# Performance work log

Hardware: AMD Instinct MI355X
Metric: run time of the kernel (lower is better)

The kernel has to match this reference:

```python
import jax, jax.numpy as jnp
import numpy as np

N, E = 20000, 320000
NODE_DIM, EDGE_DIM, EMB, HEADS, HIDDEN, OUT = 128, 16, 128, 4, 512, 64
NEG_SLOPE = 0.2


def _gatv2(x, src0, dst0, ea, Wl, bl, Wr, br, We, att, bias):
    """PyG GATv2Conv (concat=True, add_self_loops=True, fill_value='mean')."""
    n = x.shape[0]
    e = src0.shape[0]
    H, C = att.shape
    # self loops; self-loop edge_attr = mean of incoming edge_attr per node (0 if none)
    cnt = jax.ops.segment_sum(jnp.ones((e,), x.dtype), dst0, num_segments=n)
    loop_attr = jax.ops.segment_sum(ea, dst0, num_segments=n) / jnp.maximum(cnt, 1.0)[:, None]
    loops = jnp.arange(n, dtype=src0.dtype)
    src = jnp.concatenate([src0, loops])
    dst = jnp.concatenate([dst0, loops])
    ea_full = jnp.concatenate([ea, loop_attr], axis=0)
    xl = (x @ Wl + bl).reshape(n, H, C)   # source transform
    xr = (x @ Wr + br).reshape(n, H, C)   # target transform
    ef = (ea_full @ We).reshape(-1, H, C)  # edge transform (no bias in PyG)
    s = jax.nn.leaky_relu(xl[src] + xr[dst] + ef, NEG_SLOPE)  # [E', H, C]
    logits = jnp.einsum('ehc,hc->eh', s, att)
    # scatter-softmax over incoming edges of each dst node (stable)
    mx = jax.ops.segment_max(logits, dst, num_segments=n)
    num = jnp.exp(logits - mx[dst])
    den = jax.ops.segment_sum(num, dst, num_segments=n)
    alpha = num / (den[dst] + 1e-16)
    out = jax.ops.segment_sum(alpha[:, :, None] * xl[src], dst, num_segments=n)
    return out.reshape(n, H * C) + bias


def _lin(key, fan_in, fan_out, dt=jnp.float32):
    return jax.random.normal(key, (fan_in, fan_out), dt) * (1.0 / np.sqrt(fan_in))


def setup_inputs() -> dict:
    key = jax.random.key(0)
    ks = jax.random.split(key, 24)
    HC = HEADS * EMB
    inp = {
        'x': jax.random.normal(ks[0], (N, NODE_DIM), jnp.float32),
        'edge_index': jax.random.randint(ks[1], (2, E), 0, N, jnp.int64),
        'edge_attr': jax.random.normal(ks[2], (E, EDGE_DIM), jnp.float32),
        # GATv2 layer 1
        'Wl1': _lin(ks[3], NODE_DIM, HC), 'bl1': jnp.zeros((HC,), jnp.float32),
        'Wr1': _lin(ks[4], NODE_DIM, HC), 'br1': jnp.zeros((HC,), jnp.float32),
        'We1': _lin(ks[5], EDGE_DIM, HC),
        'att1': jax.random.normal(ks[6], (HEADS, EMB), jnp.float32) * (1.0 / np.sqrt(EMB)),
        'bias1': jnp.zeros((HC,), jnp.float32),
        # GATv2 layer 2
        'Wl2': _lin(ks[7], HC, HC), 'bl2': jnp.zeros((HC,), jnp.float32),
        'Wr2': _lin(ks[8], HC, HC), 'br2': jnp.zeros((HC,), jnp.float32),
        'We2': _lin(ks[9], EDGE_DIM, HC),
        'att2': jax.random.normal(ks[10], (HEADS, EMB), jnp.float32) * (1.0 / np.sqrt(EMB)),
        'bias2': jnp.zeros((HC,), jnp.float32),
        # decoder MLP
        'Wd1': _lin(ks[11], HC, HIDDEN), 'bd1': jnp.zeros((HIDDEN,), jnp.float32),
        'Wd2': _lin(ks[12], HIDDEN, OUT), 'bd2': jnp.zeros((OUT,), jnp.float32),
    }
    return inp


def reference(x, edge_index, edge_attr,
              Wl1, bl1, Wr1, br1, We1, att1, bias1,
              Wl2, bl2, Wr2, br2, We2, att2, bias2,
              Wd1, bd1, Wd2, bd2):
    src, dst = edge_index[0], edge_index[1]
    h = _gatv2(x, src, dst, edge_attr, Wl1, bl1, Wr1, br1, We1, att1, bias1)
    h = _gatv2(h, src, dst, edge_attr, Wl2, bl2, Wr2, br2, We2, att2, bias2)
    q = jax.nn.relu(h @ Wd1 + bd1) @ Wd2 + bd2
    return q
```

## Files before the change

### kernel.cpp

```cpp
#include <hip/hip_runtime.h>
#include <hip/hip_fp16.h>

typedef _Float16 half8 __attribute__((ext_vector_type(8)));
typedef _Float16 half2v __attribute__((ext_vector_type(2)));
typedef float f32x4 __attribute__((ext_vector_type(4)));

#if __has_builtin(__builtin_amdgcn_fdot2)
#define FDOT2(a, b, c) __builtin_amdgcn_fdot2((a), (b), (c), false)
#else
static __device__ __forceinline__ float FDOT2(half2v a, half2v b, float c) {
  return (float)a[0] * (float)b[0] + (float)a[1] * (float)b[1] + c;
}
#endif
#define H2(v8, p) ((half2v){(v8)[2 * (p)], (v8)[2 * (p) + 1]})

#define GLOAD_LDS16(gp, lp)                                                        \
  __builtin_amdgcn_global_load_lds(                                                \
      (const __attribute__((address_space(1))) void*)(gp),                         \
      (__attribute__((address_space(3))) void*)(lp), 16, 0, 0)

template <int CTRL>
__device__ __forceinline__ float dpp_add16(float x) {
  int y = __builtin_amdgcn_update_dpp(0, __float_as_int(x), CTRL, 0xf, 0xf, true);
  return x + __int_as_float(y);
}
__device__ __forceinline__ float rowsum16(float x) {
  x = dpp_add16<0x128>(x);
  x = dpp_add16<0x124>(x);
  x = dpp_add16<0x122>(x);
  x = dpp_add16<0x121>(x);
  return x;
}

__global__ void prep_kernel(const float* __restrict__ x, _Float16* __restrict__ x16, int nx,
                            const float* __restrict__ Wl1, const float* __restrict__ Wr1,
                            _Float16* __restrict__ WlrT1,
                            const float* __restrict__ Wl2, const float* __restrict__ Wr2,
                            _Float16* __restrict__ WlrT2,
                            const float* __restrict__ Wd1, _Float16* __restrict__ WdT1,
                            const float* __restrict__ Wd2, _Float16* __restrict__ WdT2,
                            const float* __restrict__ We1, _Float16* __restrict__ WeP1,
                            const float* __restrict__ We2, _Float16* __restrict__ WeP2) {
  int i = blockIdx.x * 256 + threadIdx.x;
  if (i < nx) { x16[i] = (_Float16)x[i]; return; }
  i -= nx;
  if (i < 1024 * 128) {
    int n = i >> 7, k = i & 127;
    float v = (n < 512) ? Wl1[(size_t)k * 512 + n] : Wr1[(size_t)k * 512 + (n - 512)];
    WlrT1[i] = (_Float16)v; return;
  }
  i -= 1024 * 128;
  if (i < 1024 * 512) {
    int n = i >> 9, k = i & 511;
    float v = (n < 512) ? Wl2[(size_t)k * 512 + n] : Wr2[(size_t)k * 512 + (n - 512)];
    WlrT2[i] = (_Float16)v; return;
  }
  i -= 1024 * 512;
  if (i < 512 * 512) { int n = i >> 9, k = i & 511; WdT1[i] = (_Float16)Wd1[(size_t)k * 512 + n]; return; }
  i -= 512 * 512;
  if (i < 64 * 512)  { int n = i >> 9, k = i & 511; WdT2[i] = (_Float16)Wd2[(size_t)k * 64 + n]; return; }
  i -= 64 * 512;
  if (i < 512 * 16)  { int c = i >> 4, k = i & 15; WeP1[i] = (_Float16)We1[(size_t)k * 512 + c]; return; }
  i -= 512 * 16;
  if (i < 512 * 16)  { int c = i >> 4, k = i & 15; WeP2[i] = (_Float16)We2[(size_t)k * 512 + c]; return; }
}

__global__ void deg_hist_kernel(const int* __restrict__ dst0, int* __restrict__ deg, int E) {
  int i = blockIdx.x * 256 + threadIdx.x;
  if (i < E) atomicAdd(&deg[dst0[i]], 1);
}

__global__ __launch_bounds__(1024) void scan_kernel(const int* __restrict__ deg, int* __restrict__ offs, int N) {
  __shared__ int part[1024];
  int t = threadIdx.x;
  int chunk = (N + 1023) / 1024;
  int b = t * chunk, e = min(b + chunk, N);
  int s = 0;
  for (int i = b; i < e; i++) s += deg[i] + 1;
  part[t] = s;
  __syncthreads();
  for (int off = 1; off < 1024; off <<= 1) {
    int v = (t >= off) ? part[t - off] : 0;
    __syncthreads();
    part[t] += v;
    __syncthreads();
  }
  int run = (t == 0) ? 0 : part[t - 1];
  for (int i = b; i < e; i++) { offs[i] = run; run += deg[i] + 1; }
  if (t == 1023) offs[N] = part[1023];
}

__global__ void csr_fill_kernel(const int* __restrict__ src0, const int* __restrict__ dst0,
                                const float* __restrict__ ea,
                                const int* __restrict__ offs, const int* __restrict__ deg,
                                int* __restrict__ cnt, int* __restrict__ csr_src,
                                _Float16* __restrict__ eas, int E, int N) {
  int i = blockIdx.x * 256 + threadIdx.x;
  if (i < 12) {
    csr_src[E + N + i] = 0;
#pragma unroll
    for (int k = 0; k < 16; k++) eas[(size_t)(E + N + i) * 16 + k] = (_Float16)0.f;
  }
  if (i < E) {
    int d = dst0[i];
    int p = offs[d] + atomicAdd(&cnt[d], 1);
    csr_src[p] = src0[i];
    const float* s = ea + (size_t)i * 16;
    half8 h0, h1;
#pragma unroll
    for (int k = 0; k < 8; k++) { h0[k] = (_Float16)s[k]; h1[k] = (_Float16)s[k + 8]; }
    *(half8*)(eas + (size_t)p * 16) = h0;
    *(half8*)(eas + (size_t)p * 16 + 8) = h1;
  } else if (i < E + N) {
    int v = i - E;
    csr_src[offs[v] + deg[v]] = v;
  }
}

__global__ void loop_attr_kernel(const int* __restrict__ offs, const int* __restrict__ deg,
                                 _Float16* __restrict__ eas, int N) {
  int i = blockIdx.x * 256 + threadIdx.x;
  if (i >= N * 16) return;
  int v = i >> 4, k = i & 15;
  int b = offs[v], dg = deg[v];
  float s = 0.f;
  for (int j = 0; j < dg; j++) s += (float)eas[((size_t)(b + j)) * 16 + k];
  eas[((size_t)(b + dg)) * 16 + k] = (_Float16)(s / fmaxf((float)dg, 1.0f));
}

template <bool RELU, bool OUT_F32>
__global__ __launch_bounds__(256) void gemm_f16(const _Float16* __restrict__ A,
                                                const _Float16* __restrict__ BT,
                                                const float* __restrict__ biasA,
                                                const float* __restrict__ biasB,
                                                void* __restrict__ C,
                                                int M, int K, int Nfull, int ldc) {
  __shared__ _Float16 As[128 * 32];
  __shared__ _Float16 Bs[128 * 32];
  int t = threadIdx.x;
  int m0 = blockIdx.x * 128;
  int n0 = blockIdx.y * 128;
  int l = t & 63, w = t >> 6;
  int wm = w & 1, wn = w >> 1;
  int lr = l & 15, lq = l >> 4;

  f32x4 acc[4][4];
#pragma unroll
  for (int i = 0; i < 4; i++)
#pragma unroll
    for (int j = 0; j < 4; j++) acc[i][j] = (f32x4){0.f, 0.f, 0.f, 0.f};

  int r0 = w * 32 + (l >> 2);
  int cb = (l & 3) * 8;
  const _Float16* Ap = A + (size_t)(m0 + r0) * K + cb;
  const _Float16* Bp = BT + (size_t)(n0 + r0) * K + cb;
  _Float16* AsW = As + w * 32 * 32;
  _Float16* BsW = Bs + w * 32 * 32;

  for (int kk = 0; kk < K; kk += 32) {
    GLOAD_LDS16(Ap, AsW);
    GLOAD_LDS16(Ap + (size_t)16 * K, AsW + 16 * 32);
    GLOAD_LDS16(Bp, BsW);
    GLOAD_LDS16(Bp + (size_t)16 * K, BsW + 16 * 32);
    Ap += 32; Bp += 32;
    __syncthreads();
    half8 af[4], bf[4];
#pragma unroll
    for (int mi = 0; mi < 4; mi++) af[mi] = *(const half8*)&As[(wm * 64 + mi * 16 + lr) * 32 + lq * 8];
#pragma unroll
    for (int ni = 0; ni < 4; ni++) bf[ni] = *(const half8*)&Bs[(wn * 64 + ni * 16 + lr) * 32 + lq * 8];
#pragma unroll
    for (int mi = 0; mi < 4; mi++)
#pragma unroll
      for (int ni = 0; ni < 4; ni++)
        acc[mi][ni] = __builtin_amdgcn_mfma_f32_16x16x32_f16(af[mi], bf[ni], acc[mi][ni], 0, 0, 0);
    __syncthreads();
  }

#pragma unroll
  for (int ni = 0; ni < 4; ni++) {
    int col = n0 + wn * 64 + ni * 16 + lr;
    if (col >= Nfull) continue;
    float bv = (col < 512) ? biasA[col] : biasB[col - 512];
#pragma unroll
    for (int mi = 0; mi < 4; mi++) {
#pragma unroll
      for (int r = 0; r < 4; r++) {
        int row = m0 + wm * 64 + mi * 16 + lq * 4 + r;
        if (row >= M) continue;
        float v = acc[mi][ni][r] + bv;
        if (RELU) v = fmaxf(v, 0.f);
        if (OUT_F32) ((float*)C)[(size_t)row * ldc + col] = v;
        else ((_Float16*)C)[(size_t)row * ldc + col] = (_Float16)v;
      }
    }
  }
}


__device__ __forceinline__ void edge_compute(
    half8 xs, half8 e0, half8 e1,
    const half8 Wf0[8], const half8 Wf1[8],
    const float attf[8], const float xrf[8],
    float& m, float& den, float acc[8]) {
  float xsf[8];
#pragma unroll
  for (int jj = 0; jj < 8; jj++) xsf[jj] = (float)xs[jj];
  float partial = 0.f;
#pragma unroll
  for (int jj = 0; jj < 8; jj++) {
    float ef = xsf[jj] + xrf[jj];
#pragma unroll
    for (int p = 0; p < 4; p++) ef = FDOT2(H2(e0, p), H2(Wf0[jj], p), ef);
#pragma unroll
    for (int p = 0; p < 4; p++) ef = FDOT2(H2(e1, p), H2(Wf1[jj], p), ef);
    float val = fmaxf(ef, 0.2f * ef);
    partial = fmaf(val, attf[jj], partial);
  }
  partial = rowsum16(partial);
  float mn = fmaxf(m, partial);
  float sc = __expf(m - mn);
  float al = __expf(partial - mn);
  den = den * sc + al;
#pragma unroll
  for (int jj = 0; jj < 8; jj++) acc[jj] = fmaf(acc[jj], sc, al * xsf[jj]);
  m = mn;
}

__global__ __launch_bounds__(256) void gat_fused_kernel(
    const _Float16* __restrict__ xlr,
    const int* __restrict__ csr_src, const int* __restrict__ offs,
    const _Float16* __restrict__ eas,
    const _Float16* __restrict__ WeP,
    const float* __restrict__ att, const float* __restrict__ bias,
    _Float16* __restrict__ hout, int N) {
  int l = threadIdx.x & 63;
  int h = l >> 4;
  int c0 = l * 8;

  half8 Wf0[8], Wf1[8];
#pragma unroll
  for (int j = 0; j < 8; j++) {
    Wf0[j] = *(const half8*)(WeP + (size_t)(c0 + j) * 16);
    Wf1[j] = *(const half8*)(WeP + (size_t)(c0 + j) * 16 + 8);
  }
  float attf[8];
  const float* attp = att + h * 128 + (l & 15) * 8;
#pragma unroll
  for (int j = 0; j < 8; j++) attf[j] = attp[j];

  int wid = blockIdx.x * 4 + (threadIdx.x >> 6);
  int nw = gridDim.x * 4;

  for (int v0 = wid; v0 < N; v0 += nw) {
    int v = __builtin_amdgcn_readfirstlane(v0);
    int b = offs[v], e2 = offs[v + 1];
    half8 xrv = *(const half8*)(xlr + (size_t)v * 1024 + 512 + c0);
    float xrf[8];
#pragma unroll
    for (int jj = 0; jj < 8; jj++) xrf[jj] = (float)xrv[jj];

    int s0 = csr_src[b], s1 = csr_src[b + 1], s2 = csr_src[b + 2];
    half8 xs0 = *(const half8*)(xlr + (size_t)s0 * 1024 + c0);
    half8 a00 = *(const half8*)(eas + (size_t)b * 16);
    half8 a01 = *(const half8*)(eas + (size_t)b * 16 + 8);
    half8 xs1 = *(const half8*)(xlr + (size_t)s1 * 1024 + c0);
    half8 a10 = *(const half8*)(eas + (size_t)(b + 1) * 16);
    half8 a11 = *(const half8*)(eas + (size_t)(b + 1) * 16 + 8);
    half8 xs2 = *(const half8*)(xlr + (size_t)s2 * 1024 + c0);
    half8 a20 = *(const half8*)(eas + (size_t)(b + 2) * 16);
    half8 a21 = *(const half8*)(eas + (size_t)(b + 2) * 16 + 8);
    int s3 = csr_src[b + 3], s4 = csr_src[b + 4], s5 = csr_src[b + 5];

    float m = -1e30f, den = 0.f;
    float acc[8];
#pragma unroll
    for (int j = 0; j < 8; j++) acc[j] = 0.f;

    for (int j = b; j < e2; j += 3) {
      edge_compute(xs0, a00, a01, Wf0, Wf1, attf, xrf, m, den, acc);
      xs0 = *(const half8*)(xlr + (size_t)s3 * 1024 + c0);
      a00 = *(const half8*)(eas + (size_t)(j + 3) * 16);
      a01 = *(const half8*)(eas + (size_t)(j + 3) * 16 + 8);
      s3 = csr_src[j + 6];
      if (j + 1 < e2)
        edge_compute(xs1, a10, a11, Wf0, Wf1, attf, xrf, m, den, acc);
      xs1 = *(const half8*)(xlr + (size_t)s4 * 1024 + c0);
      a10 = *(const half8*)(eas + (size_t)(j + 4) * 16);
      a11 = *(const half8*)(eas + (size_t)(j + 4) * 16 + 8);
      s4 = csr_src[j + 7];
      if (j + 2 < e2)
        edge_compute(xs2, a20, a21, Wf0, Wf1, attf, xrf, m, den, acc);
      xs2 = *(const half8*)(xlr + (size_t)s5 * 1024 + c0);
      a20 = *(const half8*)(eas + (size_t)(j + 5) * 16);
      a21 = *(const half8*)(eas + (size_t)(j + 5) * 16 + 8);
      s5 = csr_src[j + 8];
    }
    float rd = 1.f / (den + 1e-16f);
    half8 o;
#pragma unroll
    for (int jj = 0; jj < 8; jj++) o[jj] = (_Float16)(fmaf(acc[jj], rd, bias[c0 + jj]));
    *(half8*)(hout + (size_t)v * 512 + c0) = o;
  }
}


extern "C" void kernel_launch(void* const* d_in, const int* in_sizes, int n_in,
                              void* d_out, int out_size, void* d_ws, size_t ws_size,
                              hipStream_t stream) {
  (void)n_in; (void)out_size; (void)ws_size;
  const float* x    = (const float*)d_in[0];
  const int*   ei   = (const int*)d_in[1];
  const float* ea   = (const float*)d_in[2];
  const float* Wl1  = (const float*)d_in[3];
  const float* bl1  = (const float*)d_in[4];
  const float* Wr1  = (const float*)d_in[5];
  const float* br1  = (const float*)d_in[6];
  const float* We1  = (const float*)d_in[7];
  const float* att1 = (const float*)d_in[8];
  const float* bias1= (const float*)d_in[9];
  const float* Wl2  = (const float*)d_in[10];
  const float* bl2  = (const float*)d_in[11];
  const float* Wr2  = (const float*)d_in[12];
  const float* br2  = (const float*)d_in[13];
  const float* We2  = (const float*)d_in[14];
  const float* att2 = (const float*)d_in[15];
  const float* bias2= (const float*)d_in[16];
  const float* Wd1  = (const float*)d_in[17];
  const float* bd1  = (const float*)d_in[18];
  const float* Wd2  = (const float*)d_in[19];
  const float* bd2  = (const float*)d_in[20];

  const int N = in_sizes[0] / 128;
  const int E = in_sizes[1] / 2;
  const int EP = E + N;
  const int Npad = (N + 127) & ~127;
  const int* src0 = ei;
  const int* dst0 = ei + E;

  char* ws = (char*)d_ws;
  size_t off = 0;
  auto alloc = [&](size_t bytes) -> void* {
    void* p = ws + off;
    off += (bytes + 255) & ~(size_t)255;
    return p;
  };

  int*   deg    = (int*)alloc((size_t)N * 8);
  int*   cnt    = deg + N;
  int*   offs   = (int*)alloc(((size_t)N + 1) * 4);
  int*   csr_src= (int*)alloc(((size_t)EP + 12) * 4);
  _Float16* eas = (_Float16*)alloc(((size_t)EP + 12) * 16 * 2);
  _Float16* x16   = (_Float16*)alloc((size_t)Npad * 128 * 2);
  _Float16* xlr16 = (_Float16*)alloc((size_t)Npad * 1024 * 2);
  _Float16* h16   = (_Float16*)alloc((size_t)Npad * 512 * 2);
  _Float16* WlrT1 = (_Float16*)alloc(1024 * 128 * 2);
  _Float16* WlrT2 = (_Float16*)alloc(1024 * 512 * 2);
  _Float16* WdT1  = (_Float16*)alloc(512 * 512 * 2);
  _Float16* WdT2  = (_Float16*)alloc(128 * 512 * 2);
  _Float16* WeP1  = (_Float16*)alloc(512 * 16 * 2);
  _Float16* WeP2  = (_Float16*)alloc(512 * 16 * 2);
  _Float16* t16   = xlr16;

  hipMemsetAsync(deg, 0, (size_t)N * 8, stream);

  int nx = N * 128;
  int prep_total = nx + 1024 * 128 + 1024 * 512 + 512 * 512 + 64 * 512 + 512 * 16 + 512 * 16;
  prep_kernel<<<(prep_total + 255) / 256, 256, 0, stream>>>(
      x, x16, nx, Wl1, Wr1, WlrT1, Wl2, Wr2, WlrT2,
      Wd1, WdT1, Wd2, WdT2, We1, WeP1, We2, WeP2);

  int g;
  g = (E + 255) / 256;  deg_hist_kernel<<<g, 256, 0, stream>>>(dst0, deg, E);
  scan_kernel<<<1, 1024, 0, stream>>>(deg, offs, N);
  g = (EP + 255) / 256;
  csr_fill_kernel<<<g, 256, 0, stream>>>(src0, dst0, ea, offs, deg, cnt, csr_src, eas, E, N);
  g = (N * 16 + 255) / 256;
  loop_attr_kernel<<<g, 256, 0, stream>>>(offs, deg, eas, N);

  dim3 gb(256);
  dim3 ggm((N + 127) / 128, 8);
  dim3 ggd((N + 127) / 128, 4);
  dim3 ggo((N + 127) / 128, 1);

  const int FGRID = 2048;

  gemm_f16<false, false><<<ggm, gb, 0, stream>>>(x16, WlrT1, bl1, br1, xlr16, N, 128, 1024, 1024);
  gat_fused_kernel<<<FGRID, 256, 0, stream>>>(xlr16, csr_src, offs, eas, WeP1, att1, bias1, h16, N);

  gemm_f16<false, false><<<ggm, gb, 0, stream>>>(h16, WlrT2, bl2, br2, xlr16, N, 512, 1024, 1024);
  gat_fused_kernel<<<FGRID, 256, 0, stream>>>(xlr16, csr_src, offs, eas, WeP2, att2, bias2, h16, N);

  gemm_f16<true, false><<<ggd, gb, 0, stream>>>(h16, WdT1, bd1, bd1, t16, N, 512, 512, 512);
  gemm_f16<false, true><<<ggo, gb, 0, stream>>>(t16, WdT2, bd2, bd2, d_out, N, 512, 64, 64);
}
```

Measured before the change: 535.1 us.

## Compute GAT edge logits in packed fp16 with LDS-resident edge weights, 4-edge batches

Rewrites the fused GATv2 edge loop. Edge projection, the add, leaky-relu and the attention dot now run in packed half2 arithmetic instead of fp32 FDOT2 chains. The edge weight matrix is staged into LDS in k-major layout rather than held in 16 registers per lane, and att is converted to fp16. Edges are processed four at a time with a deeper gather prefetch, aiming to cut VALU work and register pressure. The cost is reduced precision in the logits from fp16 accumulation, plus added LDS reads.

```diff
diff --git a/kernel.cpp b/kernel.cpp
--- a/kernel.cpp
+++ b/kernel.cpp
@@ -39,8 +39,10 @@
                             _Float16* __restrict__ WlrT2,
                             const float* __restrict__ Wd1, _Float16* __restrict__ WdT1,
                             const float* __restrict__ Wd2, _Float16* __restrict__ WdT2,
-                            const float* __restrict__ We1, _Float16* __restrict__ WeP1,
-                            const float* __restrict__ We2, _Float16* __restrict__ WeP2) {
+                            const float* __restrict__ We1, _Float16* __restrict__ WeK1,
+                            const float* __restrict__ We2, _Float16* __restrict__ WeK2,
+                            const float* __restrict__ att1, _Float16* __restrict__ att16_1,
+                            const float* __restrict__ att2, _Float16* __restrict__ att16_2) {
   int i = blockIdx.x * 256 + threadIdx.x;
   if (i < nx) { x16[i] = (_Float16)x[i]; return; }
   i -= nx;
@@ -60,9 +62,13 @@
   i -= 512 * 512;
   if (i < 64 * 512)  { int n = i >> 9, k = i & 511; WdT2[i] = (_Float16)Wd2[(size_t)k * 64 + n]; return; }
   i -= 64 * 512;
-  if (i < 512 * 16)  { int c = i >> 4, k = i & 15; WeP1[i] = (_Float16)We1[(size_t)k * 512 + c]; return; }
+  if (i < 512 * 16)  { WeK1[i] = (_Float16)We1[i]; return; }
   i -= 512 * 16;
-  if (i < 512 * 16)  { int c = i >> 4, k = i & 15; WeP2[i] = (_Float16)We2[(size_t)k * 512 + c]; return; }
+  if (i < 512 * 16)  { WeK2[i] = (_Float16)We2[i]; return; }
+  i -= 512 * 16;
+  if (i < 512)       { att16_1[i] = (_Float16)att1[i]; return; }
+  i -= 512;
+  if (i < 512)       { att16_2[i] = (_Float16)att2[i]; return; }
 }
 
 __global__ void deg_hist_kernel(const int* __restrict__ dst0, int* __restrict__ deg, int E) {
@@ -198,32 +204,13 @@
 }
 
 
-__device__ __forceinline__ void edge_compute(
-    half8 xs, half8 e0, half8 e1,
-    const half8 Wf0[8], const half8 Wf1[8],
-    const float attf[8], const float xrf[8],
-    float& m, float& den, float acc[8]) {
-  float xsf[8];
-#pragma unroll
-  for (int jj = 0; jj < 8; jj++) xsf[jj] = (float)xs[jj];
-  float partial = 0.f;
-#pragma unroll
-  for (int jj = 0; jj < 8; jj++) {
-    float ef = xsf[jj] + xrf[jj];
-#pragma unroll
-    for (int p = 0; p < 4; p++) ef = FDOT2(H2(e0, p), H2(Wf0[jj], p), ef);
-#pragma unroll
-    for (int p = 0; p < 4; p++) ef = FDOT2(H2(e1, p), H2(Wf1[jj], p), ef);
-    float val = fmaxf(ef, 0.2f * ef);
-    partial = fmaf(val, attf[jj], partial);
-  }
-  partial = rowsum16(partial);
-  float mn = fmaxf(m, partial);
+__device__ __forceinline__ void upd(float p, half8 xs, float& m, float& den, float acc[8]) {
+  float mn = fmaxf(m, p);
   float sc = __expf(m - mn);
-  float al = __expf(partial - mn);
+  float al = __expf(p - mn);
   den = den * sc + al;
 #pragma unroll
-  for (int jj = 0; jj < 8; jj++) acc[jj] = fmaf(acc[jj], sc, al * xsf[jj]);
+  for (int jj = 0; jj < 8; jj++) acc[jj] = acc[jj] * sc + al * (float)xs[jj];
   m = mn;
 }
 
@@ -231,70 +218,110 @@
     const _Float16* __restrict__ xlr,
     const int* __restrict__ csr_src, const int* __restrict__ offs,
     const _Float16* __restrict__ eas,
-    const _Float16* __restrict__ WeP,
-    const float* __restrict__ att, const float* __restrict__ bias,
+    const _Float16* __restrict__ WeK,
+    const _Float16* __restrict__ att16,
+    const float* __restrict__ bias,
     _Float16* __restrict__ hout, int N) {
-  int l = threadIdx.x & 63;
+  __shared__ _Float16 WeL[16 * 512];
+  int t = threadIdx.x;
+  int l = t & 63;
+  int w = t >> 6;
   int h = l >> 4;
   int c0 = l * 8;
 
-  half8 Wf0[8], Wf1[8];
-#pragma unroll
-  for (int j = 0; j < 8; j++) {
-    Wf0[j] = *(const half8*)(WeP + (size_t)(c0 + j) * 16);
-    Wf1[j] = *(const half8*)(WeP + (size_t)(c0 + j) * 16 + 8);
-  }
-  float attf[8];
-  const float* attp = att + h * 128 + (l & 15) * 8;
-#pragma unroll
-  for (int j = 0; j < 8; j++) attf[j] = attp[j];
-
-  int wid = blockIdx.x * 4 + (threadIdx.x >> 6);
+  {
+    const _Float16* gW = WeK + w * 512 + l * 8;
+    _Float16* lW = WeL + w * 512;
+#pragma unroll
+    for (int p = 0; p < 4; p++) GLOAD_LDS16(gW + p * 2048, lW + p * 2048);
+  }
+  __syncthreads();
+
+  half8 attv = *(const half8*)(att16 + h * 128 + (l & 15) * 8);
+  const half2v lk = {(_Float16)0.2f, (_Float16)0.2f};
+
+  int wid = blockIdx.x * 4 + w;
   int nw = gridDim.x * 4;
 
   for (int v0 = wid; v0 < N; v0 += nw) {
     int v = __builtin_amdgcn_readfirstlane(v0);
     int b = offs[v], e2 = offs[v + 1];
     half8 xrv = *(const half8*)(xlr + (size_t)v * 1024 + 512 + c0);
-    float xrf[8];
-#pragma unroll
-    for (int jj = 0; jj < 8; jj++) xrf[jj] = (float)xrv[jj];
-
-    int s0 = csr_src[b], s1 = csr_src[b + 1], s2 = csr_src[b + 2];
+
+    int s0 = csr_src[b], s1 = csr_src[b + 1], s2 = csr_src[b + 2], s3 = csr_src[b + 3];
     half8 xs0 = *(const half8*)(xlr + (size_t)s0 * 1024 + c0);
-    half8 a00 = *(const half8*)(eas + (size_t)b * 16);
-    half8 a01 = *(const half8*)(eas + (size_t)b * 16 + 8);
     half8 xs1 = *(const half8*)(xlr + (size_t)s1 * 1024 + c0);
-    half8 a10 = *(const half8*)(eas + (size_t)(b + 1) * 16);
-    half8 a11 = *(const half8*)(eas + (size_t)(b + 1) * 16 + 8);
     half8 xs2 = *(const half8*)(xlr + (size_t)s2 * 1024 + c0);
-    half8 a20 = *(const half8*)(eas + (size_t)(b + 2) * 16);
-    half8 a21 = *(const half8*)(eas + (size_t)(b + 2) * 16 + 8);
-    int s3 = csr_src[b + 3], s4 = csr_src[b + 4], s5 = csr_src[b + 5];
+    half8 xs3 = *(const half8*)(xlr + (size_t)s3 * 1024 + c0);
 
     float m = -1e30f, den = 0.f;
     float acc[8];
 #pragma unroll
     for (int j = 0; j < 8; j++) acc[j] = 0.f;
 
-    for (int j = b; j < e2; j += 3) {
-      edge_compute(xs0, a00, a01, Wf0, Wf1, attf, xrf, m, den, acc);
-      xs0 = *(const half8*)(xlr + (size_t)s3 * 1024 + c0);
-      a00 = *(const half8*)(eas + (size_t)(j + 3) * 16);
-      a01 = *(const half8*)(eas + (size_t)(j + 3) * 16 + 8);
-      s3 = csr_src[j + 6];
-      if (j + 1 < e2)
-        edge_compute(xs1, a10, a11, Wf0, Wf1, attf, xrf, m, den, acc);
-      xs1 = *(const half8*)(xlr + (size_t)s4 * 1024 + c0);
-      a10 = *(const half8*)(eas + (size_t)(j + 4) * 16);
-      a11 = *(const half8*)(eas + (size_t)(j + 4) * 16 + 8);
-      s4 = csr_src[j + 7];
-      if (j + 2 < e2)
-        edge_compute(xs2, a20, a21, Wf0, Wf1, attf, xrf, m, den, acc);
-      xs2 = *(const half8*)(xlr + (size_t)s5 * 1024 + c0);
-      a20 = *(const half8*)(eas + (size_t)(j + 5) * 16);
-      a21 = *(const half8*)(eas + (size_t)(j + 5) * 16 + 8);
-      s5 = csr_src[j + 8];
+    for (int j = b; j < e2; j += 4) {
+      half8 x0 = xs0, x1 = xs1, x2 = xs2, x3 = xs3;
+      int n0 = csr_src[j + 4], n1 = csr_src[j + 5], n2 = csr_src[j + 6], n3 = csr_src[j + 7];
+      xs0 = *(const half8*)(xlr + (size_t)n0 * 1024 + c0);
+      xs1 = *(const half8*)(xlr + (size_t)n1 * 1024 + c0);
+      xs2 = *(const half8*)(xlr + (size_t)n2 * 1024 + c0);
+      xs3 = *(const half8*)(xlr + (size_t)n3 * 1024 + c0);
+      const half8 a00 = *(const half8*)(eas + (size_t)(j + 0) * 16);
+      const half8 a01 = *(const half8*)(eas + (size_t)(j + 0) * 16 + 8);
+      const half8 a10 = *(const half8*)(eas + (size_t)(j + 1) * 16);
+      const half8 a11 = *(const half8*)(eas + (size_t)(j + 1) * 16 + 8);
+      const half8 a20 = *(const half8*)(eas + (size_t)(j + 2) * 16);
+      const half8 a21 = *(const half8*)(eas + (size_t)(j + 2) * 16 + 8);
+      const half8 a30 = *(const half8*)(eas + (size_t)(j + 3) * 16);
+      const half8 a31 = *(const half8*)(eas + (size_t)(j + 3) * 16 + 8);
+
+      half2v e0[4], e1[4], e2v[4], e3[4];
+#pragma unroll
+      for (int p = 0; p < 4; p++) {
+        e0[p] = (half2v){0, 0}; e1[p] = (half2v){0, 0};
+        e2v[p] = (half2v){0, 0}; e3[p] = (half2v){0, 0};
+      }
+#pragma unroll
+      for (int k = 0; k < 16; k++) {
+        half8 wr = *(const half8*)(WeL + k * 512 + c0);
+        _Float16 q0 = (k < 8) ? a00[k] : a01[k - 8];
+        _Float16 q1 = (k < 8) ? a10[k] : a11[k - 8];
+        _Float16 q2 = (k < 8) ? a20[k] : a21[k - 8];
+        _Float16 q3 = (k < 8) ? a30[k] : a31[k - 8];
+        half2v k0 = {q0, q0}, k1 = {q1, q1}, k2 = {q2, q2}, k3 = {q3, q3};
+#pragma unroll
+        for (int p = 0; p < 4; p++) {
+          half2v wp = H2(wr, p);
+          e0[p] += k0 * wp;
+          e1[p] += k1 * wp;
+          e2v[p] += k2 * wp;
+          e3[p] += k3 * wp;
+        }
+      }
+      float p0 = 0.f, p1 = 0.f, p2 = 0.f, p3 = 0.f;
+#pragma unroll
+      for (int p = 0; p < 4; p++) {
+        half2v xrp = H2(xrv, p);
+        half2v ap = H2(attv, p);
+        half2v v0 = H2(x0, p) + xrp + e0[p];
+        half2v v1 = H2(x1, p) + xrp + e1[p];
+        half2v v2 = H2(x2, p) + xrp + e2v[p];
+        half2v v3 = H2(x3, p) + xrp + e3[p];
+        v0 = __builtin_elementwise_max(v0, v0 * lk);
+        v1 = __builtin_elementwise_max(v1, v1 * lk);
+        v2 = __builtin_elementwise_max(v2, v2 * lk);
+        v3 = __builtin_elementwise_max(v3, v3 * lk);
+        p0 = FDOT2(v0, ap, p0);
+        p1 = FDOT2(v1, ap, p1);
+        p2 = FDOT2(v2, ap, p2);
+        p3 = FDOT2(v3, ap, p3);
+      }
+      p0 = rowsum16(p0); p1 = rowsum16(p1); p2 = rowsum16(p2); p3 = rowsum16(p3);
+
+      upd(p0, x0, m, den, acc);
+      if (j + 1 < e2) upd(p1, x1, m, den, acc);
+      if (j + 2 < e2) upd(p2, x2, m, den, acc);
+      if (j + 3 < e2) upd(p3, x3, m, den, acc);
     }
     float rd = 1.f / (den + 1e-16f);
     half8 o;
@@ -358,17 +385,21 @@
   _Float16* WlrT2 = (_Float16*)alloc(1024 * 512 * 2);
   _Float16* WdT1  = (_Float16*)alloc(512 * 512 * 2);
   _Float16* WdT2  = (_Float16*)alloc(128 * 512 * 2);
-  _Float16* WeP1  = (_Float16*)alloc(512 * 16 * 2);
-  _Float16* WeP2  = (_Float16*)alloc(512 * 16 * 2);
+  _Float16* WeK1  = (_Float16*)alloc(16 * 512 * 2);
+  _Float16* WeK2  = (_Float16*)alloc(16 * 512 * 2);
+  _Float16* att16_1 = (_Float16*)alloc(512 * 2);
+  _Float16* att16_2 = (_Float16*)alloc(512 * 2);
   _Float16* t16   = xlr16;
 
   hipMemsetAsync(deg, 0, (size_t)N * 8, stream);
 
   int nx = N * 128;
-  int prep_total = nx + 1024 * 128 + 1024 * 512 + 512 * 512 + 64 * 512 + 512 * 16 + 512 * 16;
+  int prep_total = nx + 1024 * 128 + 1024 * 512 + 512 * 512 + 64 * 512
+                 + 512 * 16 + 512 * 16 + 512 + 512;
   prep_kernel<<<(prep_total + 255) / 256, 256, 0, stream>>>(
       x, x16, nx, Wl1, Wr1, WlrT1, Wl2, Wr2, WlrT2,
-      Wd1, WdT1, Wd2, WdT2, We1, WeP1, We2, WeP2);
+      Wd1, WdT1, Wd2, WdT2, We1, WeK1, We2, WeK2,
+      att1, att16_1, att2, att16_2);
 
   int g;
   g = (E + 255) / 256;  deg_hist_kernel<<<g, 256, 0, stream>>>(dst0, deg, E);
@@ -386,10 +417,10 @@
   const int FGRID = 2048;
 
   gemm_f16<false, false><<<ggm, gb, 0, stream>>>(x16, WlrT1, bl1, br1, xlr16, N, 128, 1024, 1024);
-  gat_fused_kernel<<<FGRID, 256, 0, stream>>>(xlr16, csr_src, offs, eas, WeP1, att1, bias1, h16, N);
+  gat_fused_kernel<<<FGRID, 256, 0, stream>>>(xlr16, csr_src, offs, eas, WeK1, att16_1, bias1, h16, N);
 
   gemm_f16<false, false><<<ggm, gb, 0, stream>>>(h16, WlrT2, bl2, br2, xlr16, N, 512, 1024, 1024);
-  gat_fused_kernel<<<FGRID, 256, 0, stream>>>(xlr16, csr_src, offs, eas, WeP2, att2, bias2, h16, N);
+  gat_fused_kernel<<<FGRID, 256, 0, stream>>>(xlr16, csr_src, offs, eas, WeK2, att16_2, bias2, h16, N);
 
   gemm_f16<true, false><<<ggd, gb, 0, stream>>>(h16, WdT1, bd1, bd1, t16, N, 512, 512, 512);
   gemm_f16<false, true><<<ggo, gb, 0, stream>>>(t16, WdT2, bd2, bd2, d_out, N, 512, 64, 64);
```

New measurement: 539.3 us. No clear change (+0.8%).
